# Kernel optimization log

Hardware: AMD Instinct MI355X
Metric: run time of the kernel (lower is better)

The kernel has to match this reference:

```python
import jax, jax.numpy as jnp
import numpy as np

L = 8        # num_layers
B = 4        # batch
S = 1024     # seq_len
D = 1024     # hidden_size
H = 16       # num_heads
FC = 4096    # fc_size
NEG = -1e9   # additive causal-mask value (matches torch code's -1000000000.0)


def setup_inputs() -> dict:
    key = jax.random.key(0)
    ks = jax.random.split(key, 12)
    std = 0.02
    inputs = jax.random.normal(ks[0], (B, S, D), jnp.float32)
    # per-layer stacked parameters; torch Linear y = x W^T + b, here stored as [in, out]
    Wq = jax.random.normal(ks[1], (L, D, D), jnp.float32) * std
    Wk = jax.random.normal(ks[2], (L, D, D), jnp.float32) * std
    Wv = jax.random.normal(ks[3], (L, D, D), jnp.float32) * std
    Wo = jax.random.normal(ks[4], (L, D, D), jnp.float32) * std
    W1 = jax.random.normal(ks[5], (L, D, FC), jnp.float32) * std
    W2 = jax.random.normal(ks[6], (L, FC, D), jnp.float32) * std
    bq = jnp.zeros((L, D), jnp.float32)
    bk = jnp.zeros((L, D), jnp.float32)
    bv = jnp.zeros((L, D), jnp.float32)
    bo = jnp.zeros((L, D), jnp.float32)
    b1 = jnp.zeros((L, FC), jnp.float32)
    b2 = jnp.zeros((L, D), jnp.float32)
    ln_g = jnp.ones((D,), jnp.float32)   # single LayerNorm shared across all sites
    ln_b = jnp.zeros((D,), jnp.float32)
    scale = jnp.asarray(0.1, jnp.float32)  # re-zero residual scale (init 0 in torch; 0.1 for non-degenerate test)
    return dict(inputs=inputs, Wq=Wq, bq=bq, Wk=Wk, bk=bk, Wv=Wv, bv=bv,
                Wo=Wo, bo=bo, W1=W1, b1=b1, W2=W2, b2=b2,
                ln_g=ln_g, ln_b=ln_b, scale=scale)


def reference(inputs, Wq, bq, Wk, bk, Wv, bv, Wo, bo, W1, b1, W2, b2, ln_g, ln_b, scale):
    Bz, Sl, Dm = inputs.shape
    nL = Wq.shape[0]
    dh = Dm // H
    inv_sqrt_dh = 1.0 / np.sqrt(dh).astype(np.float32)

    def layer_norm(x):  # shared gamma/beta, eps matches torch default 1e-5
        mu = jnp.mean(x, axis=-1, keepdims=True)
        var = jnp.var(x, axis=-1, keepdims=True)
        return (x - mu) * jax.lax.rsqrt(var + 1e-5) * ln_g + ln_b

    # causal additive bias [S, S], broadcasts over [B, H, S, S]
    bias = jnp.triu(jnp.full((Sl, Sl), NEG, inputs.dtype), k=1)

    x = inputs
    for i in range(nL):
        # --- masked self-attention block ---
        r = layer_norm(x)
        q = (r @ Wq[i] + bq[i]).reshape(Bz, Sl, H, dh)
        k = (r @ Wk[i] + bk[i]).reshape(Bz, Sl, H, dh)
        v = (r @ Wv[i] + bv[i]).reshape(Bz, Sl, H, dh)
        logits = jnp.einsum('bqhd,bkhd->bhqk', q, k) * inv_sqrt_dh + bias
        attn = jax.nn.softmax(logits, axis=-1)
        vals = jnp.einsum('bhqk,bkhd->bqhd', attn, v).reshape(Bz, Sl, Dm)
        r = vals @ Wo[i] + bo[i]
        x = x + scale * r  # re-zero residual (dropout is identity at inference)
        # --- FFN block ---
        r = layer_norm(x)
        r = jax.nn.gelu(r @ W1[i] + b1[i], approximate=False) @ W2[i] + b2[i]
        x = x + scale * r
    return layer_norm(x)
```

## Files before the change

### kernel.cpp

```cpp
#include <hip/hip_runtime.h>


typedef __bf16 bf16x8 __attribute__((ext_vector_type(8)));
typedef float  f32x4  __attribute__((ext_vector_type(4)));

#define DEV static __device__ __forceinline__

DEV unsigned short f2bf(float x) {
  unsigned u = __builtin_bit_cast(unsigned int, x);
  u += 0x7fffu + ((u >> 16) & 1u);
  return (unsigned short)(u >> 16);
}

DEV f32x4 mfma16(bf16x8 a, bf16x8 b, f32x4 c) {
  return __builtin_amdgcn_mfma_f32_16x16x32_bf16(a, b, c, 0, 0, 0);
}

DEV bf16x8 ldb8(const unsigned short* p) {
  return *reinterpret_cast<const bf16x8*>(p);
}

DEV void gload_lds16(const unsigned short* g, unsigned short* l) {
  __builtin_amdgcn_global_load_lds(
      (const __attribute__((address_space(1))) void*)g,
      (__attribute__((address_space(3))) void*)l, 16, 0, 0);
}

__global__ void transpose_cvt(const float* __restrict__ src,
                              unsigned short* __restrict__ dst,
                              int srcStride, int dstStride) {
  __shared__ float tile[32][33];
  const int t  = threadIdx.x;
  const int r  = t >> 3;
  const int c4 = (t & 7) << 2;
  const int k  = blockIdx.x * 32 + r;
  const int n0 = blockIdx.y * 32 + c4;
  const float4 v = *reinterpret_cast<const float4*>(src + (size_t)k * srcStride + n0);
  tile[r][c4] = v.x; tile[r][c4 + 1] = v.y; tile[r][c4 + 2] = v.z; tile[r][c4 + 3] = v.w;
  __syncthreads();
  const int n  = blockIdx.y * 32 + r;
  const int k0 = blockIdx.x * 32 + c4;
  ushort4 o;
  o.x = f2bf(tile[c4][r]);     o.y = f2bf(tile[c4 + 1][r]);
  o.z = f2bf(tile[c4 + 2][r]); o.w = f2bf(tile[c4 + 3][r]);
  *reinterpret_cast<ushort4*>(dst + (size_t)n * dstStride + k0) = o;
}

__global__ void transpose_cvt4(const float* __restrict__ Wq, const float* __restrict__ Wk,
                               const float* __restrict__ Wv, const float* __restrict__ Wo,
                               unsigned short* __restrict__ Wqkv_t,
                               unsigned short* __restrict__ Wo_t) {
  __shared__ float tile[32][33];
  const int z = blockIdx.z;
  const float* src = (z == 0) ? Wq : (z == 1) ? Wk : (z == 2) ? Wv : Wo;
  unsigned short* dst = (z == 3) ? Wo_t : (Wqkv_t + (size_t)z * 1024 * 1024);
  const int t  = threadIdx.x;
  const int r  = t >> 3;
  const int c4 = (t & 7) << 2;
  const int k  = blockIdx.x * 32 + r;
  const int n0 = blockIdx.y * 32 + c4;
  const float4 v = *reinterpret_cast<const float4*>(src + (size_t)k * 1024 + n0);
  tile[r][c4] = v.x; tile[r][c4 + 1] = v.y; tile[r][c4 + 2] = v.z; tile[r][c4 + 3] = v.w;
  __syncthreads();
  const int n  = blockIdx.y * 32 + r;
  const int k0 = blockIdx.x * 32 + c4;
  ushort4 o;
  o.x = f2bf(tile[c4][r]);     o.y = f2bf(tile[c4 + 1][r]);
  o.z = f2bf(tile[c4 + 2][r]); o.w = f2bf(tile[c4 + 3][r]);
  *reinterpret_cast<ushort4*>(dst + (size_t)n * 1024 + k0) = o;
}

__global__ void pack_qkv_bias(const float* __restrict__ bq, const float* __restrict__ bk,
                              const float* __restrict__ bv, float* __restrict__ out) {
  int i = blockIdx.x * 256 + threadIdx.x;
  out[i] = (i < 1024) ? bq[i] : (i < 2048 ? bk[i - 1024] : bv[i - 2048]);
}

template <int OUTF32>
__global__ void ln_kernel(const float* x, const float* __restrict__ gam,
                          const float* __restrict__ bet, void* out) {
  const int row = blockIdx.x;
  const int t   = threadIdx.x;
  const float* xr = x + (size_t)row * 1024;
  const float4 v = *reinterpret_cast<const float4*>(xr + t * 4);
  float s  = v.x + v.y + v.z + v.w;
  float ss = v.x * v.x + v.y * v.y + v.z * v.z + v.w * v.w;
  #pragma unroll
  for (int m = 32; m; m >>= 1) { s += __shfl_xor(s, m); ss += __shfl_xor(ss, m); }
  __shared__ float red[8];
  const int wv = t >> 6, ln = t & 63;
  if (ln == 0) { red[wv] = s; red[4 + wv] = ss; }
  __syncthreads();
  s  = red[0] + red[1] + red[2] + red[3];
  ss = red[4] + red[5] + red[6] + red[7];
  const float mean = s * (1.0f / 1024.0f);
  const float var  = ss * (1.0f / 1024.0f) - mean * mean;
  const float rstd = rsqrtf(var + 1e-5f);
  const float4 g  = *reinterpret_cast<const float4*>(gam + t * 4);
  const float4 bb = *reinterpret_cast<const float4*>(bet + t * 4);
  const float y0 = (v.x - mean) * rstd * g.x + bb.x;
  const float y1 = (v.y - mean) * rstd * g.y + bb.y;
  const float y2 = (v.z - mean) * rstd * g.z + bb.z;
  const float y3 = (v.w - mean) * rstd * g.w + bb.w;
  if (OUTF32) {
    float4 o; o.x = y0; o.y = y1; o.z = y2; o.w = y3;
    *reinterpret_cast<float4*>((float*)out + (size_t)row * 1024 + t * 4) = o;
  } else {
    ushort4 o; o.x = f2bf(y0); o.y = f2bf(y1); o.z = f2bf(y2); o.w = f2bf(y3);
    *reinterpret_cast<ushort4*>((unsigned short*)out + (size_t)row * 1024 + t * 4) = o;
  }
}

template <int MODE, int BN>
__global__ __launch_bounds__(256) void gemm2(
    const unsigned short* __restrict__ A, const unsigned short* __restrict__ Bt,
    const float* __restrict__ bias, unsigned short* __restrict__ outb,
    const float* xin, float* xout, const float* __restrict__ scale_p,
    unsigned short* __restrict__ vT, int N, int K) {
  constexpr int NI = BN / 32;
  constexpr int BSH = BN * 64;
  __shared__ __attribute__((aligned(16))) unsigned short lds[2][8192 + BSH];
  const int t = threadIdx.x, wave = t >> 6, lane = t & 63;
  const int m0 = blockIdx.x * 128, n0 = blockIdx.y * BN;
  const int wm = wave >> 1, wn = wave & 1;

  int srowA[4], scolA[4];
  #pragma unroll
  for (int j = 0; j < 4; ++j) {
    const int c = j * 256 + wave * 64 + lane;
    const int r = c >> 3;
    srowA[j] = r;
    scolA[j] = ((c & 7) ^ (r & 7)) << 3;
  }
  const unsigned short* aBase = A + (size_t)m0 * K;
  const unsigned short* bBase = Bt + (size_t)n0 * K;

  const int xk0 = (((lane >> 4)    ) ^ (lane & 7)) << 3;
  const int xk1 = (((lane >> 4) | 4) ^ (lane & 7)) << 3;
  const int arow = (wm * 64 + (lane & 15)) * 64;
  const int brow = (wn * (BN / 2) + (lane & 15)) * 64;

  f32x4 acc[4][NI] = {};
  const int nk = K >> 6;
  constexpr int BJ = NI;

  {
    unsigned short* l = &lds[0][0];
    #pragma unroll
    for (int j = 0; j < 4; ++j)
      gload_lds16(aBase + (size_t)srowA[j] * K + scolA[j], l + j * 2048 + wave * 512);
    #pragma unroll
    for (int j = 0; j < BJ; ++j)
      gload_lds16(bBase + (size_t)srowA[j] * K + scolA[j], l + 8192 + j * 2048 + wave * 512);
  }
  __syncthreads();

  int cur = 0;
  for (int kt = 0; kt < nk; ++kt) {
    if (kt + 1 < nk) {
      unsigned short* l = &lds[cur ^ 1][0];
      const int ko = (kt + 1) * 64;
      #pragma unroll
      for (int j = 0; j < 4; ++j)
        gload_lds16(aBase + (size_t)srowA[j] * K + ko + scolA[j], l + j * 2048 + wave * 512);
      #pragma unroll
      for (int j = 0; j < BJ; ++j)
        gload_lds16(bBase + (size_t)srowA[j] * K + ko + scolA[j], l + 8192 + j * 2048 + wave * 512);
    }
    const unsigned short* l = &lds[cur][0];
    #pragma unroll
    for (int kc = 0; kc < 2; ++kc) {
      const int xk = kc ? xk1 : xk0;
      bf16x8 a[4], b[NI];
      #pragma unroll
      for (int mi = 0; mi < 4; ++mi) a[mi] = ldb8(&l[arow + mi * 1024 + xk]);
      #pragma unroll
      for (int ni = 0; ni < NI; ++ni) b[ni] = ldb8(&l[8192 + brow + ni * 1024 + xk]);
      __builtin_amdgcn_s_setprio(1);
      #pragma unroll
      for (int mi = 0; mi < 4; ++mi)
        #pragma unroll
        for (int ni = 0; ni < NI; ++ni)
          acc[mi][ni] = mfma16(a[mi], b[ni], acc[mi][ni]);
      __builtin_amdgcn_s_setprio(0);
    }
    __syncthreads();
    cur ^= 1;
  }

  const int mrow = m0 + wm * 64 + (lane >> 4) * 4;
  const int ncol = n0 + wn * (BN / 2) + (lane & 15);
  float scl = 0.f;
  if constexpr (MODE == 2) scl = scale_p[0];
  #pragma unroll
  for (int ni = 0; ni < NI; ++ni) {
    const int n = ncol + ni * 16;
    const float bn = bias[n];
    #pragma unroll
    for (int mi = 0; mi < 4; ++mi) {
      const int row0 = mrow + mi * 16;
      if constexpr (MODE == 3) {
        if (n >= 2048) {
          const int h = (n - 2048) >> 6, d = (n - 2048) & 63;
          const int b = row0 >> 10, s = row0 & 1023;
          ushort4 o;
          o.x = f2bf(acc[mi][ni][0] + bn); o.y = f2bf(acc[mi][ni][1] + bn);
          o.z = f2bf(acc[mi][ni][2] + bn); o.w = f2bf(acc[mi][ni][3] + bn);
          *reinterpret_cast<ushort4*>(vT + ((size_t)(b * 16 + h) * 64 + d) * 1024 + s) = o;
          continue;
        }
      }
      #pragma unroll
      for (int r = 0; r < 4; ++r) {
        const size_t idx = (size_t)(row0 + r) * N + n;
        float v = acc[mi][ni][r] + bn;
        if constexpr (MODE == 1) {
          v = 0.5f * v * (1.0f + erff(v * 0.70710678118f));
          outb[idx] = f2bf(v);
        } else if constexpr (MODE == 2) {
          xout[idx] = xin[idx] + scl * v;
        } else {
          outb[idx] = f2bf(v);
        }
      }
    }
  }
}

__global__ __launch_bounds__(256) void attn_kernel(
    const unsigned short* __restrict__ qkv, const unsigned short* __restrict__ vT,
    unsigned short* __restrict__ vals) {
  const int bh = blockIdx.x & 63;
  const int g  = 15 - (blockIdx.x >> 6);
  const int b = bh >> 4, h = bh & 15;
  const int t = threadIdx.x, wave = t >> 6, lane = t & 63;
  const int rowLane = lane & 15, grp = lane >> 4;
  const int qt = g * 4 + wave;
  const int q0 = qt * 16;
  const int nkt = (qt >> 2) + 1;

  __shared__ __attribute__((aligned(16))) unsigned short P_lds[4][16 * 72];
  unsigned short* P = P_lds[wave];

  const unsigned short* qkvB  = qkv + (size_t)b * 1024 * 3072;
  const unsigned short* kBase = qkvB + 1024 + h * 64 + grp * 8;
  const unsigned short* vHead = vT + (size_t)bh * 64 * 1024;

  const unsigned short* qb = qkvB + (size_t)(q0 + rowLane) * 3072 + h * 64 + grp * 8;
  const bf16x8 aq0 = ldb8(qb);
  const bf16x8 aq1 = ldb8(qb + 32);

  f32x4 oacc[4] = {};
  float mrun[4], lrun[4];
  #pragma unroll
  for (int r = 0; r < 4; ++r) { mrun[r] = -1e30f; lrun[r] = 0.f; }

  bf16x8 k0[4], k1[4];
  #pragma unroll
  for (int nf = 0; nf < 4; ++nf) {
    const unsigned short* kb = kBase + (size_t)(nf * 16 + rowLane) * 3072;
    k0[nf] = ldb8(kb); k1[nf] = ldb8(kb + 32);
  }

  for (int kt = 0; kt < nkt; ++kt) {
    const int kv0 = kt * 64;
    bf16x8 v0[4], v1[4];
    #pragma unroll
    for (int df = 0; df < 4; ++df) {
      const unsigned short* vb = vHead + (size_t)(df * 16 + rowLane) * 1024 + kv0 + grp * 8;
      v0[df] = ldb8(vb); v1[df] = ldb8(vb + 32);
    }
    f32x4 sacc[4];
    #pragma unroll
    for (int nf = 0; nf < 4; ++nf) {
      f32x4 z = {0.f, 0.f, 0.f, 0.f};
      z = mfma16(aq0, k0[nf], z);
      z = mfma16(aq1, k1[nf], z);
      sacc[nf] = z;
    }
    if (kt + 1 < nkt) {
      #pragma unroll
      for (int nf = 0; nf < 4; ++nf) {
        const unsigned short* kb = kBase + (size_t)(kv0 + 64 + nf * 16 + rowLane) * 3072;
        k0[nf] = ldb8(kb); k1[nf] = ldb8(kb + 32);
      }
    }
    float pl[4][4], mx[4];
    #pragma unroll
    for (int r = 0; r < 4; ++r) {
      #pragma unroll
      for (int nf = 0; nf < 4; ++nf) pl[nf][r] = sacc[nf][r] * 0.125f;
    }
    if (kt == nkt - 1) {
      #pragma unroll
      for (int r = 0; r < 4; ++r) {
        const int qg = q0 + grp * 4 + r;
        #pragma unroll
        for (int nf = 0; nf < 4; ++nf)
          if (kv0 + nf * 16 + rowLane > qg) pl[nf][r] = -1e30f;
      }
    }
    #pragma unroll
    for (int r = 0; r < 4; ++r)
      mx[r] = fmaxf(fmaxf(pl[0][r], pl[1][r]), fmaxf(pl[2][r], pl[3][r]));
    #pragma unroll
    for (int m = 1; m <= 8; m <<= 1)
      #pragma unroll
      for (int r = 0; r < 4; ++r) mx[r] = fmaxf(mx[r], __shfl_xor(mx[r], m));
    float fac[4], rs[4];
    #pragma unroll
    for (int r = 0; r < 4; ++r) {
      const float mnew = fmaxf(mrun[r], mx[r]);
      fac[r] = __expf(mrun[r] - mnew);
      mrun[r] = mnew;
      float acc = 0.f;
      #pragma unroll
      for (int nf = 0; nf < 4; ++nf) {
        const float e = __expf(pl[nf][r] - mnew);
        pl[nf][r] = e;
        acc += e;
      }
      rs[r] = acc;
    }
    #pragma unroll
    for (int m = 1; m <= 8; m <<= 1)
      #pragma unroll
      for (int r = 0; r < 4; ++r) rs[r] += __shfl_xor(rs[r], m);
    #pragma unroll
    for (int r = 0; r < 4; ++r) lrun[r] = lrun[r] * fac[r] + rs[r];
    #pragma unroll
    for (int df = 0; df < 4; ++df)
      #pragma unroll
      for (int r = 0; r < 4; ++r) oacc[df][r] *= fac[r];
    #pragma unroll
    for (int nf = 0; nf < 4; ++nf)
      #pragma unroll
      for (int r = 0; r < 4; ++r)
        P[(grp * 4 + r) * 72 + nf * 16 + rowLane] = f2bf(pl[nf][r]);
    const bf16x8 pa0 = ldb8(&P[rowLane * 72 + grp * 8]);
    const bf16x8 pa1 = ldb8(&P[rowLane * 72 + 32 + grp * 8]);
    #pragma unroll
    for (int df = 0; df < 4; ++df) {
      oacc[df] = mfma16(pa0, v0[df], oacc[df]);
      oacc[df] = mfma16(pa1, v1[df], oacc[df]);
    }
  }
  float rl[4];
  #pragma unroll
  for (int r = 0; r < 4; ++r) rl[r] = 1.0f / lrun[r];
  #pragma unroll
  for (int df = 0; df < 4; ++df)
    #pragma unroll
    for (int r = 0; r < 4; ++r) {
      const int qg = q0 + grp * 4 + r;
      const float v = oacc[df][r] * rl[r];
      vals[(size_t)(b * 1024 + qg) * 1024 + h * 64 + df * 16 + rowLane] = f2bf(v);
    }
}

extern "C" void kernel_launch(void* const* d_in, const int* in_sizes, int n_in,
                              void* d_out, int out_size, void* d_ws, size_t ws_size,
                              hipStream_t stream) {
  (void)in_sizes; (void)n_in; (void)out_size; (void)ws_size;
  const float* inputs = (const float*)d_in[0];
  const float* Wq = (const float*)d_in[1];  const float* bq = (const float*)d_in[2];
  const float* Wk = (const float*)d_in[3];  const float* bk = (const float*)d_in[4];
  const float* Wv = (const float*)d_in[5];  const float* bv = (const float*)d_in[6];
  const float* Wo = (const float*)d_in[7];  const float* bo = (const float*)d_in[8];
  const float* W1 = (const float*)d_in[9];  const float* b1 = (const float*)d_in[10];
  const float* W2 = (const float*)d_in[11]; const float* b2 = (const float*)d_in[12];
  const float* ln_g = (const float*)d_in[13];
  const float* ln_b = (const float*)d_in[14];
  const float* scale_p = (const float*)d_in[15];
  float* xbuf = (float*)d_out;

  char* w = (char*)d_ws;
  size_t off = 0;
  auto take = [&](size_t bytes) {
    void* p = w + off;
    off = (off + bytes + 255) & ~(size_t)255;
    return p;
  };
  unsigned short* Wqkv_t = (unsigned short*)take((size_t)3072 * 1024 * 2);
  unsigned short* Wo_t   = (unsigned short*)take((size_t)1024 * 1024 * 2);
  unsigned short* W1_t   = (unsigned short*)take((size_t)4096 * 1024 * 2);
  unsigned short* W2_t   = (unsigned short*)take((size_t)1024 * 4096 * 2);
  float*          bqkv   = (float*)take(3072 * 4);
  unsigned short* rbuf   = (unsigned short*)take((size_t)4096 * 1024 * 2);
  unsigned short* qkvb   = (unsigned short*)take((size_t)4096 * 3072 * 2);
  unsigned short* vTb    = (unsigned short*)take((size_t)64 * 64 * 1024 * 2);
  unsigned short* valsb  = (unsigned short*)take((size_t)4096 * 1024 * 2);
  unsigned short* hbuf   = (unsigned short*)take((size_t)4096 * 4096 * 2);

  for (int i = 0; i < 8; ++i) {
    const float* xin = (i == 0) ? inputs : xbuf;
    transpose_cvt4<<<dim3(32, 32, 4), 256, 0, stream>>>(
        Wq + (size_t)i * 1024 * 1024, Wk + (size_t)i * 1024 * 1024,
        Wv + (size_t)i * 1024 * 1024, Wo + (size_t)i * 1024 * 1024, Wqkv_t, Wo_t);
    transpose_cvt<<<dim3(32, 128), 256, 0, stream>>>(W1 + (size_t)i * 1024 * 4096, W1_t, 4096, 1024);
    transpose_cvt<<<dim3(128, 32), 256, 0, stream>>>(W2 + (size_t)i * 4096 * 1024, W2_t, 1024, 4096);
    pack_qkv_bias<<<12, 256, 0, stream>>>(bq + i * 1024, bk + i * 1024, bv + i * 1024, bqkv);
    ln_kernel<0><<<4096, 256, 0, stream>>>(xin, ln_g, ln_b, rbuf);
    gemm2<3, 128><<<dim3(32, 24), 256, 0, stream>>>(rbuf, Wqkv_t, bqkv, qkvb,
                                                    nullptr, nullptr, nullptr, vTb, 3072, 1024);
    attn_kernel<<<1024, 256, 0, stream>>>(qkvb, vTb, valsb);
    gemm2<2, 64><<<dim3(32, 16), 256, 0, stream>>>(valsb, Wo_t, bo + i * 1024, nullptr,
                                                   xin, xbuf, scale_p, nullptr, 1024, 1024);
    ln_kernel<0><<<4096, 256, 0, stream>>>(xbuf, ln_g, ln_b, rbuf);
    gemm2<1, 128><<<dim3(32, 32), 256, 0, stream>>>(rbuf, W1_t, b1 + i * 4096, hbuf,
                                                    nullptr, nullptr, nullptr, nullptr, 4096, 1024);
    gemm2<2, 64><<<dim3(32, 16), 256, 0, stream>>>(hbuf, W2_t, b2 + i * 1024, nullptr,
                                                   xbuf, xbuf, scale_p, nullptr, 1024, 4096);
  }
  ln_kernel<1><<<4096, 256, 0, stream>>>(xbuf, ln_g, ln_b, xbuf);
}
```

Baseline: 2.134 ms.

## Split attention KV range into two chunks with a separate merge kernel

```diff
diff --git a/kernel.cpp b/kernel.cpp
--- a/kernel.cpp
+++ b/kernel.cpp
@@ -25,6 +25,10 @@
       (const __attribute__((address_space(1))) void*)g,
       (__attribute__((address_space(3))) void*)l, 16, 0, 0);
 }
+
+__constant__ unsigned char attn_zmap[32] = {
+    14, 15, 31, 12, 13, 29, 30, 10, 11, 27, 28, 8, 9, 25, 26,
+    6, 7, 23, 24, 4, 5, 21, 22, 2, 3, 19, 20, 0, 1, 17, 18, 16};
 
 __global__ void transpose_cvt(const float* __restrict__ src,
                               unsigned short* __restrict__ dst,
@@ -229,15 +233,19 @@
 
 __global__ __launch_bounds__(256) void attn_kernel(
     const unsigned short* __restrict__ qkv, const unsigned short* __restrict__ vT,
-    unsigned short* __restrict__ vals) {
+    float* __restrict__ opart, float* __restrict__ oml) {
   const int bh = blockIdx.x & 63;
-  const int g  = 15 - (blockIdx.x >> 6);
+  const int cg = attn_zmap[blockIdx.x >> 6];
+  const int c  = cg >> 4, g = cg & 15;
   const int b = bh >> 4, h = bh & 15;
   const int t = threadIdx.x, wave = t >> 6, lane = t & 63;
   const int rowLane = lane & 15, grp = lane >> 4;
   const int qt = g * 4 + wave;
   const int q0 = qt * 16;
-  const int nkt = (qt >> 2) + 1;
+  const int nkt = g + 1;
+  const int half = (nkt + 1) >> 1;
+  const int k0   = c ? half : 0;
+  const int kend = c ? nkt : half;
 
   __shared__ __attribute__((aligned(16))) unsigned short P_lds[4][16 * 72];
   unsigned short* P = P_lds[wave];
@@ -255,14 +263,16 @@
   #pragma unroll
   for (int r = 0; r < 4; ++r) { mrun[r] = -1e30f; lrun[r] = 0.f; }
 
-  bf16x8 k0[4], k1[4];
-  #pragma unroll
-  for (int nf = 0; nf < 4; ++nf) {
-    const unsigned short* kb = kBase + (size_t)(nf * 16 + rowLane) * 3072;
-    k0[nf] = ldb8(kb); k1[nf] = ldb8(kb + 32);
-  }
-
-  for (int kt = 0; kt < nkt; ++kt) {
+  bf16x8 k0f[4], k1f[4];
+  if (k0 < kend) {
+    #pragma unroll
+    for (int nf = 0; nf < 4; ++nf) {
+      const unsigned short* kb = kBase + (size_t)(k0 * 64 + nf * 16 + rowLane) * 3072;
+      k0f[nf] = ldb8(kb); k1f[nf] = ldb8(kb + 32);
+    }
+  }
+
+  for (int kt = k0; kt < kend; ++kt) {
     const int kv0 = kt * 64;
     bf16x8 v0[4], v1[4];
     #pragma unroll
@@ -274,15 +284,15 @@
     #pragma unroll
     for (int nf = 0; nf < 4; ++nf) {
       f32x4 z = {0.f, 0.f, 0.f, 0.f};
-      z = mfma16(aq0, k0[nf], z);
-      z = mfma16(aq1, k1[nf], z);
+      z = mfma16(aq0, k0f[nf], z);
+      z = mfma16(aq1, k1f[nf], z);
       sacc[nf] = z;
     }
-    if (kt + 1 < nkt) {
+    if (kt + 1 < kend) {
       #pragma unroll
       for (int nf = 0; nf < 4; ++nf) {
         const unsigned short* kb = kBase + (size_t)(kv0 + 64 + nf * 16 + rowLane) * 3072;
-        k0[nf] = ldb8(kb); k1[nf] = ldb8(kb + 32);
+        k0f[nf] = ldb8(kb); k1f[nf] = ldb8(kb + 32);
       }
     }
     float pl[4][4], mx[4];
@@ -345,17 +355,37 @@
       oacc[df] = mfma16(pa1, v1[df], oacc[df]);
     }
   }
-  float rl[4];
   #pragma unroll
-  for (int r = 0; r < 4; ++r) rl[r] = 1.0f / lrun[r];
-  #pragma unroll
-  for (int df = 0; df < 4; ++df)
-    #pragma unroll
-    for (int r = 0; r < 4; ++r) {
-      const int qg = q0 + grp * 4 + r;
-      const float v = oacc[df][r] * rl[r];
-      vals[(size_t)(b * 1024 + qg) * 1024 + h * 64 + df * 16 + rowLane] = f2bf(v);
-    }
+  for (int r = 0; r < 4; ++r) {
+    const int qg = q0 + grp * 4 + r;
+    const size_t row = (size_t)(c * 65536) + bh * 1024 + qg;
+    #pragma unroll
+    for (int df = 0; df < 4; ++df)
+      opart[row * 64 + df * 16 + rowLane] = oacc[df][r];
+    if (rowLane == 0) {
+      oml[row * 2]     = mrun[r];
+      oml[row * 2 + 1] = lrun[r];
+    }
+  }
+}
+
+__global__ void attn_merge(const float* __restrict__ opart, const float* __restrict__ oml,
+                           unsigned short* __restrict__ vals) {
+  const int t = threadIdx.x;
+  const int d = t & 63;
+  for (int row = blockIdx.x * 4 + (t >> 6); row < 65536; row += gridDim.x * 4) {
+    const float m0 = oml[(size_t)row * 2],           l0 = oml[(size_t)row * 2 + 1];
+    const float m1 = oml[(size_t)(65536 + row) * 2], l1 = oml[(size_t)(65536 + row) * 2 + 1];
+    const float mm = fmaxf(m0, m1);
+    const float e0 = __expf(m0 - mm), e1 = __expf(m1 - mm);
+    const float denom = l0 * e0 + l1 * e1;
+    const float o0 = opart[(size_t)row * 64 + d];
+    const float o1 = opart[(size_t)(65536 + row) * 64 + d];
+    const float v = (o0 * e0 + o1 * e1) / denom;
+    const int bh = row >> 10, s = row & 1023;
+    const int b = bh >> 4, h = bh & 15;
+    vals[(size_t)(b * 1024 + s) * 1024 + h * 64 + d] = f2bf(v);
+  }
 }
 
 extern "C" void kernel_launch(void* const* d_in, const int* in_sizes, int n_in,
@@ -391,6 +421,8 @@
   unsigned short* vTb    = (unsigned short*)take((size_t)64 * 64 * 1024 * 2);
   unsigned short* valsb  = (unsigned short*)take((size_t)4096 * 1024 * 2);
   unsigned short* hbuf   = (unsigned short*)take((size_t)4096 * 4096 * 2);
+  float*          oml    = (float*)take((size_t)2 * 65536 * 2 * 4);
+  float*          opart  = (float*)hbuf;
 
   for (int i = 0; i < 8; ++i) {
     const float* xin = (i == 0) ? inputs : xbuf;
@@ -403,7 +435,8 @@
     ln_kernel<0><<<4096, 256, 0, stream>>>(xin, ln_g, ln_b, rbuf);
     gemm2<3, 128><<<dim3(32, 24), 256, 0, stream>>>(rbuf, Wqkv_t, bqkv, qkvb,
                                                     nullptr, nullptr, nullptr, vTb, 3072, 1024);
-    attn_kernel<<<1024, 256, 0, stream>>>(qkvb, vTb, valsb);
+    attn_kernel<<<2048, 256, 0, stream>>>(qkvb, vTb, opart, oml);
+    attn_merge<<<2048, 256, 0, stream>>>(opart, oml, valsb);
     gemm2<2, 64><<<dim3(32, 16), 256, 0, stream>>>(valsb, Wo_t, bo + i * 1024, nullptr,
                                                    xin, xbuf, scale_p, nullptr, 1024, 1024);
     ln_kernel<0><<<4096, 256, 0, stream>>>(xbuf, ln_g, ln_b, rbuf);
```

Result: slower. 2.186 ms (+2.4%).

## Add 256x256-tile 8-wave GEMM with rotating LDS ring for QKV and FFN-up

Applied to the files above, without the earlier changes.

```diff
diff --git a/kernel.cpp b/kernel.cpp
--- a/kernel.cpp
+++ b/kernel.cpp
@@ -111,6 +111,113 @@
   }
 }
 
+template <int MODE>
+__global__ __launch_bounds__(512) void gemm8r(
+    const unsigned short* __restrict__ A, const unsigned short* __restrict__ Bt,
+    const float* __restrict__ bias, unsigned short* __restrict__ outb,
+    unsigned short* __restrict__ vT, int N, int K) {
+  __shared__ __attribute__((aligned(16))) unsigned short lds[7 * 8192];
+  const int t = threadIdx.x, wave = t >> 6, lane = t & 63;
+  const int wm = wave >> 2, wn = wave & 3;
+  const int rl15 = lane & 15;
+
+  const int nbn = N >> 8;
+  const int qq  = gridDim.x >> 3;
+  const int swz = (blockIdx.x & 7) * qq + (blockIdx.x >> 3);
+  const int m0 = (swz / nbn) << 8, n0 = (swz % nbn) << 8;
+
+  const unsigned short* aG = A  + (size_t)m0 * K;
+  const unsigned short* bG = Bt + (size_t)n0 * K;
+
+  const int srow = lane >> 2;
+  const int ssl  = (((lane & 3) ^ ((srow >> 1) & 3)) << 3);
+  const int swA  = (((lane >> 4) ^ ((lane >> 1) & 3)) << 3);
+
+  auto stageA = [&](int slot, int kt) {
+    #pragma unroll
+    for (int j = 0; j < 2; ++j) {
+      const int c = wave + j * 8;
+      gload_lds16(aG + (size_t)(c * 16 + srow) * K + kt * 32 + ssl,
+                  &lds[slot * 8192 + c * 512]);
+    }
+  };
+  auto stageB = [&](int slot, int kt) {
+    #pragma unroll
+    for (int j = 0; j < 2; ++j) {
+      const int c = wave + j * 8;
+      gload_lds16(bG + (size_t)(c * 16 + srow) * K + kt * 32 + ssl,
+                  &lds[slot * 8192 + c * 512]);
+    }
+  };
+
+  const int nk = K >> 5;
+  stageA(0, 0); stageB(1, 0);
+  stageA(2, 1); stageB(3, 1);
+  asm volatile("s_waitcnt vmcnt(4)" ::: "memory");
+  asm volatile("s_barrier" ::: "memory");
+
+  f32x4 acc[8][4] = {};
+  int sA = 0, sB = 1, pA = 4, pB = 5;
+
+  for (int kt = 0; kt < nk; ++kt) {
+    const bool more = (kt + 2 < nk);
+    if (more) { stageA(pA, kt + 2); stageB(pB, kt + 2); }
+    const int ab = sA * 8192, bb = sB * 8192;
+    bf16x8 af[8], bfr[4];
+    #pragma unroll
+    for (int mi = 0; mi < 8; ++mi)
+      af[mi] = ldb8(&lds[ab + (wm * 128 + mi * 16 + rl15) * 32 + swA]);
+    #pragma unroll
+    for (int ni = 0; ni < 4; ++ni)
+      bfr[ni] = ldb8(&lds[bb + (wn * 64 + ni * 16 + rl15) * 32 + swA]);
+    __builtin_amdgcn_s_setprio(1);
+    #pragma unroll
+    for (int mi = 0; mi < 8; ++mi)
+      #pragma unroll
+      for (int ni = 0; ni < 4; ++ni)
+        acc[mi][ni] = mfma16(af[mi], bfr[ni], acc[mi][ni]);
+    __builtin_amdgcn_s_setprio(0);
+    if (more) asm volatile("s_waitcnt vmcnt(4)" ::: "memory");
+    else      asm volatile("s_waitcnt vmcnt(0)" ::: "memory");
+    asm volatile("s_barrier" ::: "memory");
+    sA += 2; if (sA >= 7) sA -= 7;
+    sB += 2; if (sB >= 7) sB -= 7;
+    pA += 2; if (pA >= 7) pA -= 7;
+    pB += 2; if (pB >= 7) pB -= 7;
+  }
+
+  const int mrow = m0 + wm * 128 + (lane >> 4) * 4;
+  const int ncol = n0 + wn * 64 + rl15;
+  #pragma unroll
+  for (int ni = 0; ni < 4; ++ni) {
+    const int n = ncol + ni * 16;
+    const float bn = bias[n];
+    #pragma unroll
+    for (int mi = 0; mi < 8; ++mi) {
+      const int row0 = mrow + mi * 16;
+      if constexpr (MODE == 3) {
+        if (n >= 2048) {
+          const int h = (n - 2048) >> 6, d = (n - 2048) & 63;
+          const int b = row0 >> 10, s = row0 & 1023;
+          ushort4 o;
+          o.x = f2bf(acc[mi][ni][0] + bn); o.y = f2bf(acc[mi][ni][1] + bn);
+          o.z = f2bf(acc[mi][ni][2] + bn); o.w = f2bf(acc[mi][ni][3] + bn);
+          *reinterpret_cast<ushort4*>(vT + ((size_t)(b * 16 + h) * 64 + d) * 1024 + s) = o;
+          continue;
+        }
+      }
+      #pragma unroll
+      for (int r = 0; r < 4; ++r) {
+        const size_t idx = (size_t)(row0 + r) * N + n;
+        float v = acc[mi][ni][r] + bn;
+        if constexpr (MODE == 1)
+          v = 0.5f * v * (1.0f + erff(v * 0.70710678118f));
+        outb[idx] = f2bf(v);
+      }
+    }
+  }
+}
+
 template <int MODE, int BN>
 __global__ __launch_bounds__(256) void gemm2(
     const unsigned short* __restrict__ A, const unsigned short* __restrict__ Bt,
@@ -401,14 +508,12 @@
     transpose_cvt<<<dim3(128, 32), 256, 0, stream>>>(W2 + (size_t)i * 4096 * 1024, W2_t, 1024, 4096);
     pack_qkv_bias<<<12, 256, 0, stream>>>(bq + i * 1024, bk + i * 1024, bv + i * 1024, bqkv);
     ln_kernel<0><<<4096, 256, 0, stream>>>(xin, ln_g, ln_b, rbuf);
-    gemm2<3, 128><<<dim3(32, 24), 256, 0, stream>>>(rbuf, Wqkv_t, bqkv, qkvb,
-                                                    nullptr, nullptr, nullptr, vTb, 3072, 1024);
+    gemm8r<3><<<192, 512, 0, stream>>>(rbuf, Wqkv_t, bqkv, qkvb, vTb, 3072, 1024);
     attn_kernel<<<1024, 256, 0, stream>>>(qkvb, vTb, valsb);
     gemm2<2, 64><<<dim3(32, 16), 256, 0, stream>>>(valsb, Wo_t, bo + i * 1024, nullptr,
                                                    xin, xbuf, scale_p, nullptr, 1024, 1024);
     ln_kernel<0><<<4096, 256, 0, stream>>>(xbuf, ln_g, ln_b, rbuf);
-    gemm2<1, 128><<<dim3(32, 32), 256, 0, stream>>>(rbuf, W1_t, b1 + i * 4096, hbuf,
-                                                    nullptr, nullptr, nullptr, nullptr, 4096, 1024);
+    gemm8r<1><<<256, 512, 0, stream>>>(rbuf, W1_t, b1 + i * 4096, hbuf, nullptr, 4096, 1024);
     gemm2<2, 64><<<dim3(32, 16), 256, 0, stream>>>(hbuf, W2_t, b2 + i * 1024, nullptr,
                                                    xbuf, xbuf, scale_p, nullptr, 1024, 4096);
   }
```

Result: no change. 2.104 ms (-1.4%).
